# Kernel tuning notes

Measured on AMD Instinct MI355X. Metric: run time of the kernel, lower is better.

## Reference

```python
import jax, jax.numpy as jnp
import numpy as np

B, N, D, H, K, L, BLOCKS = 8, 256, 768, 12, 128, 4, 2
HD = D // H
SCALING = HD ** -0.5
NEG = -1e9  # stand-in for -inf; exp underflows to exactly 0 in softmax


def layernorm(x, s, b):
    m = x.mean(-1, keepdims=True)
    v = ((x - m) ** 2).mean(-1, keepdims=True)
    return (x - m) * jax.lax.rsqrt(v + 1e-5) * s + b


def _gauss(x, mean, std):
    a = (2.0 * 3.14159) ** 0.5
    return jnp.exp(-0.5 * ((x - mean) / std) ** 2) / (a * std)


def setup_inputs() -> dict:
    key = jax.random.key(0)
    ks = jax.random.split(key, 16)
    nrm = lambda k, shape: jax.random.normal(k, shape, jnp.float32) * 0.02
    atoms = jax.random.randint(ks[0], (B, N), 0, 10, dtype=jnp.int32)
    pos = jax.random.normal(ks[1], (B, N, 3), jnp.float32)
    atom_emb = nrm(ks[2], (10, D)).at[0].set(0.0)  # padding_idx=0
    gbf_means = jax.random.uniform(ks[3], (K,), jnp.float32, 0.0, 3.0)
    gbf_stds = jax.random.uniform(ks[4], (K,), jnp.float32, 0.0, 3.0)
    gbf_mul = jnp.ones((100, 1), jnp.float32)
    gbf_bias = jnp.zeros((100, 1), jnp.float32)
    bp_w1 = nrm(ks[5], (K, K)); bp_b1 = jnp.zeros((K,), jnp.float32)
    bp_w2 = nrm(ks[6], (K, H)); bp_b2 = jnp.zeros((H,), jnp.float32)
    edge_w = nrm(ks[7], (K, D)); edge_b = jnp.zeros((D,), jnp.float32)
    ap_w = nrm(ks[8], (D, D)); ap_b = jnp.zeros((D,), jnp.float32)
    ln1_s = jnp.ones((L, D), jnp.float32); ln1_b = jnp.zeros((L, D), jnp.float32)
    wi = nrm(ks[9], (L, D, 3 * D)); bi = jnp.zeros((L, 3 * D), jnp.float32)
    wo = nrm(ks[10], (L, D, D)); bo = jnp.zeros((L, D), jnp.float32)
    ln2_s = jnp.ones((L, D), jnp.float32); ln2_b = jnp.zeros((L, D), jnp.float32)
    w1 = nrm(ks[11], (L, D, D)); b1 = jnp.zeros((L, D), jnp.float32)
    w2 = nrm(ks[12], (L, D, D)); b2 = jnp.zeros((L, D), jnp.float32)
    fln_s = jnp.ones((D,), jnp.float32); fln_b = jnp.zeros((D,), jnp.float32)
    return dict(atoms=atoms, pos=pos, atom_emb=atom_emb, gbf_means=gbf_means,
                gbf_stds=gbf_stds, gbf_mul=gbf_mul, gbf_bias=gbf_bias,
                bp_w1=bp_w1, bp_b1=bp_b1, bp_w2=bp_w2, bp_b2=bp_b2,
                edge_w=edge_w, edge_b=edge_b, ap_w=ap_w, ap_b=ap_b,
                ln1_s=ln1_s, ln1_b=ln1_b, wi=wi, bi=bi, wo=wo, bo=bo,
                ln2_s=ln2_s, ln2_b=ln2_b, w1=w1, b1=b1, w2=w2, b2=b2,
                fln_s=fln_s, fln_b=fln_b)


def reference(atoms, pos, atom_emb, gbf_means, gbf_stds, gbf_mul, gbf_bias,
              bp_w1, bp_b1, bp_w2, bp_b2, edge_w, edge_b, ap_w, ap_b,
              ln1_s, ln1_b, wi, bi, wo, bo, ln2_s, ln2_b, w1, b1, w2, b2,
              fln_s, fln_b):
    pad = atoms == 0  # [B,N]
    delta = pos[:, None, :, :] - pos[:, :, None, :]  # [B,N,N,3]
    sq = (delta * delta).sum(-1)
    dist = jnp.where(sq > 0, jnp.sqrt(jnp.where(sq > 0, sq, 1.0)), 0.0)  # safe sqrt
    et = atoms[:, :, None] * 10 + atoms[:, None, :]  # [B,N,N] in [0,100)
    e = gbf_mul[et] * dist[..., None] + gbf_bias[et]  # [B,N,N,1]
    gbf = _gauss(e, gbf_means, jnp.abs(gbf_stds) + 1e-5)  # [B,N,N,K]
    # zero out padded j-columns, sum over j -> per-node edge feature
    ef = jnp.where(pad[:, None, :, None], 0.0, gbf).sum(axis=2)  # [B,N,K]
    node = atom_emb[atoms] + ef @ edge_w + edge_b  # [B,N,D]
    x = jnp.swapaxes(node, 0, 1) @ ap_w + ap_b  # [N,B,D]
    # attention bias: K-dim Gaussian features -> per-head bias
    bias = jax.nn.gelu(gbf @ bp_w1 + bp_b1, approximate=False) @ bp_w2 + bp_b2  # [B,N,N,H]
    bias = jnp.transpose(bias, (0, 3, 1, 2))  # [B,H,N,N]
    bias = jnp.where(pad[:, None, None, :], NEG, bias)

    def body(x, p):
        s1, c1, Wi, Bi, Wo, Bo, s2, c2, W1, B1, W2, B2 = p
        h = layernorm(x, s1, c1)
        q, k, v = jnp.split(h @ Wi + Bi, 3, axis=-1)
        q = q.reshape(N, B, H, HD) * SCALING
        k = k.reshape(N, B, H, HD)
        v = v.reshape(N, B, H, HD)
        sc = jnp.einsum('ibhd,jbhd->bhij', q, k) + bias
        pA = jax.nn.softmax(sc, axis=-1)
        o = jnp.einsum('bhij,jbhd->ibhd', pA, v).reshape(N, B, D)
        x = x + o @ Wo + Bo
        h = layernorm(x, s2, c2)
        h = jax.nn.gelu(h @ W1 + B1, approximate=False) @ W2 + B2
        return x + h, None

    stacked = (ln1_s, ln1_b, wi, bi, wo, bo, ln2_s, ln2_b, w1, b1, w2, b2)
    for _ in range(BLOCKS):
        x, _ = jax.lax.scan(body, x, stacked)
    x = layernorm(x, fln_s, fln_b)
    return jnp.swapaxes(x, 0, 1)  # [B,N,D]
```

## Files before the change

### kernel.cpp

```cpp
#include <hip/hip_runtime.h>
#include <math.h>

constexpr int Bn = 8, Nn = 256, Dn = 768, Hn = 12, Kn = 128;
constexpr int Tn = Nn * Bn;
constexpr float SCALE = 0.125f;
constexpr float NEGB = -1e9f;

typedef __attribute__((ext_vector_type(8))) short bf16x8;
typedef __attribute__((ext_vector_type(4))) float f32x4;

#define MFMA16(a, b, c) __builtin_amdgcn_mfma_f32_16x16x32_bf16((a), (b), (c), 0, 0, 0)

__device__ __forceinline__ void gload_lds16(const void* g, void* l) {
  __builtin_amdgcn_global_load_lds(
      (const __attribute__((address_space(1))) void*)g,
      (__attribute__((address_space(3))) void*)l, 16, 0, 0);
}

__device__ __forceinline__ ushort f2bf(float x) {
  union { float f; unsigned u; } v; v.f = x;
  unsigned r = (v.u + 0x7fff + ((v.u >> 16) & 1)) >> 16;
  return (ushort)r;
}
__device__ __forceinline__ ushort f2bf_t(float x) {
  union { float f; unsigned u; } v; v.f = x;
  return (ushort)(v.u >> 16);
}
__device__ __forceinline__ float bf2f(ushort u) {
  union { unsigned u; float f; } v; v.u = ((unsigned)u) << 16;
  return v.f;
}
__device__ __forceinline__ float gelu_fast(float x) {
  float u = x * (0.7978845608f + 0.0356774081f * x * x);
  float e = __expf(2.0f * u);
  float t = 1.0f - 2.0f / (e + 1.0f);
  return 0.5f * x * (1.0f + t);
}
__device__ __forceinline__ float wave_sum(float v) {
#pragma unroll
  for (int off = 32; off; off >>= 1) v += __shfl_xor(v, off);
  return v;
}

__global__ __launch_bounds__(256) void wtrans(const float* __restrict__ W,
                                              ushort* __restrict__ WT,
                                              int Kd, int Nd) {
  __shared__ float tile[64][65];
  const float* Wl = W + (size_t)blockIdx.z * Kd * Nd;
  ushort* WTl = WT + (size_t)blockIdx.z * Kd * Nd;
  int n0 = blockIdx.x * 64, k0 = blockIdx.y * 64;
  int tid = threadIdx.x;
  for (int e = tid; e < 64 * 64; e += 256) {
    int r = e >> 6, c = e & 63;
    tile[r][c] = Wl[(size_t)(k0 + r) * Nd + n0 + c];
  }
  __syncthreads();
  for (int e = tid; e < 64 * 64; e += 256) {
    int r = e >> 6, c = e & 63;
    WTl[(size_t)(n0 + r) * Kd + k0 + c] = f2bf(tile[c][r]);
  }
}

__global__ __launch_bounds__(128) void ef_kernel(
    const int* __restrict__ atoms, const float* __restrict__ pos,
    const float* __restrict__ means, const float* __restrict__ stds,
    const float* __restrict__ gmul, const float* __restrict__ gbias,
    float* __restrict__ ef) {
  int i = blockIdx.x, b = blockIdx.y;
  __shared__ float dist[Nn], ml[Nn], bs2[Nn];
  __shared__ int padm[Nn];
  int tid = threadIdx.x;
  int ai = atoms[b * Nn + i];
  float px = pos[(b * Nn + i) * 3], py = pos[(b * Nn + i) * 3 + 1], pz = pos[(b * Nn + i) * 3 + 2];
  for (int j = tid; j < Nn; j += 128) {
    int aj = atoms[b * Nn + j];
    float dx = px - pos[(b * Nn + j) * 3];
    float dy = py - pos[(b * Nn + j) * 3 + 1];
    float dz = pz - pos[(b * Nn + j) * 3 + 2];
    float sq = dx * dx + dy * dy + dz * dz;
    dist[j] = sq > 0.f ? sqrtf(sq) : 0.f;
    int et = ai * 10 + aj;
    ml[j] = gmul[et];
    bs2[j] = gbias[et];
    padm[j] = (aj == 0);
  }
  __syncthreads();
  int k = tid;
  float mean = means[k];
  float sd = fabsf(stds[k]) + 1e-5f;
  float inv = 1.0f / sd;
  float cn = 1.0f / (sqrtf(2.0f * 3.14159f) * sd);
  float acc = 0.f;
  for (int j = 0; j < Nn; ++j) {
    if (padm[j]) continue;
    float t = (ml[j] * dist[j] + bs2[j] - mean) * inv;
    acc += __expf(-0.5f * t * t);
  }
  ef[(b * Nn + i) * Kn + k] = acc * cn;
}

__global__ __launch_bounds__(256) void gbias_kernel(
    const int* __restrict__ atoms, const float* __restrict__ pos,
    const float* __restrict__ means, const float* __restrict__ stds,
    const float* __restrict__ gmul, const float* __restrict__ gbias_,
    const ushort* __restrict__ w1T, const float* __restrict__ b1,
    const float* __restrict__ w2, const float* __restrict__ b2,
    ushort* __restrict__ biasb) {
  int i = blockIdx.x, b = blockIdx.y;
  __shared__ char W1s[32768];
  __shared__ char Ag[16384];
  __shared__ char W2s[4096];
  __shared__ float sj[256];
  __shared__ int pml[256];
  __shared__ float b1s[128], invs_[128], mui[128], cns[128];
  const int tid = threadIdx.x, w = tid >> 6, ln = tid & 63;
  const int frow = ln & 15, fgrp = ln >> 4;
  {
    int srow = ln >> 4, sc = ln & 15;
#pragma unroll
    for (int q = 0; q < 8; ++q) {
      int inst = w * 8 + q;
      int row = inst * 4 + srow;
      const char* g = (const char*)(w1T + row * 128) + ((sc * 16) ^ ((row & 7) << 4));
      gload_lds16(g, W1s + inst * 1024);
    }
  }
  if (tid < 128) {
    float mean = means[tid];
    float sd = fabsf(stds[tid]) + 1e-5f;
    float inv = 1.0f / sd;
    invs_[tid] = inv;
    mui[tid] = mean * inv;
    cns[tid] = inv * 0.3989423f;
    b1s[tid] = b1[tid];
  }
  for (int e = tid; e < 2048; e += 256) {
    int h = e >> 7, k = e & 127;
    float v = (h < 12) ? w2[k * 12 + h] : 0.f;
    *(ushort*)(W2s + h * 256 + ((2 * k) ^ ((h & 7) << 4))) = f2bf(v);
  }
  {
    int ai = atoms[b * Nn + i];
    int j = tid;
    int aj = atoms[b * Nn + j];
    float dx = pos[(b * Nn + i) * 3]     - pos[(b * Nn + j) * 3];
    float dy = pos[(b * Nn + i) * 3 + 1] - pos[(b * Nn + j) * 3 + 1];
    float dz = pos[(b * Nn + i) * 3 + 2] - pos[(b * Nn + j) * 3 + 2];
    float sq = dx * dx + dy * dy + dz * dz;
    float d = sq > 0.f ? sqrtf(sq) : 0.f;
    int et = ai * 10 + aj;
    sj[j] = fmaf(gmul[et], d, gbias_[et]);
    pml[j] = (aj == 0);
  }
  __syncthreads();

  for (int jt = 0; jt < 4; ++jt) {
    int j0 = jt * 64;
    {
      int k = tid & 127;
      float inv = invs_[k], mu = mui[k], cn = cns[k];
      int r0 = (tid >> 7) * 32;
#pragma unroll 8
      for (int rr = 0; rr < 32; ++rr) {
        int row = r0 + rr;
        float t = fmaf(inv, sj[j0 + row], -mu);
        float g = __expf(-0.5f * t * t) * cn;
        *(ushort*)(Ag + row * 256 + ((2 * k) ^ ((row & 7) << 4))) = f2bf_t(g);
      }
    }
    __syncthreads();
    f32x4 acc[8] = {};
    const int arow = w * 16 + frow;
#pragma unroll
    for (int ks = 0; ks < 4; ++ks) {
      bf16x8 af = *(const bf16x8*)(Ag + arow * 256 + ((ks * 64 + fgrp * 16) ^ ((arow & 7) << 4)));
#pragma unroll
      for (int nt = 0; nt < 8; ++nt) {
        int brow = nt * 16 + frow;
        bf16x8 bfv = *(const bf16x8*)(W1s + brow * 256 + ((ks * 64 + fgrp * 16) ^ ((brow & 7) << 4)));
        acc[nt] = MFMA16(af, bfv, acc[nt]);
      }
    }
    __syncthreads();
#pragma unroll
    for (int nt = 0; nt < 8; ++nt) {
      int n = nt * 16 + frow;
#pragma unroll
      for (int r = 0; r < 4; ++r) {
        int jloc = w * 16 + fgrp * 4 + r;
        float g = gelu_fast(acc[nt][r] + b1s[n]);
        *(ushort*)(Ag + jloc * 256 + ((2 * n) ^ ((jloc & 7) << 4))) = f2bf_t(g);
      }
    }
    __syncthreads();
    {
      f32x4 acc2 = {};
      int jrow = w * 16 + frow;
#pragma unroll
      for (int ks = 0; ks < 4; ++ks) {
        bf16x8 af = *(const bf16x8*)(Ag + jrow * 256 + ((ks * 64 + fgrp * 16) ^ ((jrow & 7) << 4)));
        bf16x8 bfv = *(const bf16x8*)(W2s + frow * 256 + ((ks * 64 + fgrp * 16) ^ ((frow & 7) << 4)));
        acc2 = MFMA16(af, bfv, acc2);
      }
      if (frow < 12) {
        float bv = b2[frow];
#pragma unroll
        for (int r = 0; r < 4; ++r) {
          int jl = w * 16 + fgrp * 4 + r;
          int jg = j0 + jl;
          float v = pml[jg] ? NEGB : (acc2[r] + bv);
          biasb[(((size_t)b * Hn + frow) * Nn + i) * Nn + jg] = f2bf(v);
        }
      }
    }
    __syncthreads();
  }
}

__global__ __launch_bounds__(256) void node_kernel(
    const int* __restrict__ atoms, const float* __restrict__ ef,
    const float* __restrict__ emb, const float* __restrict__ ew,
    const float* __restrict__ eb, ushort* __restrict__ nodeT) {
  int n = blockIdx.x, b = blockIdx.y;
  __shared__ float efs[Kn];
  int tid = threadIdx.x;
  if (tid < Kn) efs[tid] = ef[(b * Nn + n) * Kn + tid];
  __syncthreads();
  int a = atoms[b * Nn + n];
  for (int d = tid; d < Dn; d += 256) {
    float acc = emb[a * Dn + d] + eb[d];
#pragma unroll 8
    for (int k = 0; k < Kn; ++k) acc += efs[k] * ew[k * Dn + d];
    nodeT[(size_t)(b * Nn + n) * Dn + d] = f2bf(acc);
  }
}

template <int MODE>
__global__ __launch_bounds__(256, 4) void mgemm(
    const ushort* __restrict__ A, const ushort* __restrict__ WT,
    const float* __restrict__ bias, const float* __restrict__ res,
    void* __restrict__ Cout, int M, int Kd, int Nd) {
  __shared__ char smem[16384];
  char* ldsA = smem;
  char* ldsB = smem + 8192;
  const int tid = threadIdx.x, w = tid >> 6, ln = tid & 63;
  const int m0 = blockIdx.y * 64, n0 = blockIdx.x * 64;
  const int wm = (w >> 1) * 32, wn = (w & 1) * 32;
  const int srow = ln >> 3, schunk = ln & 7;
  const int sswz = (schunk * 16) ^ (srow << 4);
  const int frow = ln & 15, fgrp = ln >> 4;
  f32x4 acc[2][2] = {};
  for (int kt = 0; kt < Kd; kt += 64) {
    __syncthreads();
#pragma unroll
    for (int q = 0; q < 2; ++q) {
      int r = (w * 2 + q) * 8 + srow;
      gload_lds16((const char*)(A + (size_t)(m0 + r) * Kd + kt) + sswz, ldsA + (w * 2 + q) * 1024);
    }
#pragma unroll
    for (int q = 0; q < 2; ++q) {
      int r = (w * 2 + q) * 8 + srow;
      gload_lds16((const char*)(WT + (size_t)(n0 + r) * Kd + kt) + sswz, ldsB + (w * 2 + q) * 1024);
    }
    __syncthreads();
#pragma unroll
    for (int ks = 0; ks < 2; ++ks) {
      bf16x8 af[2], bfv[2];
#pragma unroll
      for (int mt = 0; mt < 2; ++mt) {
        int row = wm + mt * 16 + frow;
        af[mt] = *(const bf16x8*)(ldsA + row * 128 + ((ks * 64 + fgrp * 16) ^ ((row & 7) << 4)));
      }
#pragma unroll
      for (int nt = 0; nt < 2; ++nt) {
        int row = wn + nt * 16 + frow;
        bfv[nt] = *(const bf16x8*)(ldsB + row * 128 + ((ks * 64 + fgrp * 16) ^ ((row & 7) << 4)));
      }
      acc[0][0] = MFMA16(af[0], bfv[0], acc[0][0]);
      acc[0][1] = MFMA16(af[0], bfv[1], acc[0][1]);
      acc[1][0] = MFMA16(af[1], bfv[0], acc[1][0]);
      acc[1][1] = MFMA16(af[1], bfv[1], acc[1][1]);
    }
  }
#pragma unroll
  for (int nt = 0; nt < 2; ++nt) {
    int n = n0 + wn + nt * 16 + frow;
    float bv = bias[n];
#pragma unroll
    for (int mt = 0; mt < 2; ++mt) {
#pragma unroll
      for (int r = 0; r < 4; ++r) {
        int m = m0 + wm + mt * 16 + fgrp * 4 + r;
        float v = acc[mt][nt][r] + bv;
        if (MODE == 1) v = gelu_fast(v);
        if (MODE == 2) v += res[(size_t)m * Nd + n];
        if (MODE <= 1) ((ushort*)Cout)[(size_t)m * Nd + n] = f2bf(v);
        else           ((float*)Cout)[(size_t)m * Nd + n] = v;
      }
    }
  }
}

template <int MODE>
__global__ __launch_bounds__(256, 2) void mgemm128(
    const ushort* __restrict__ A, const ushort* __restrict__ WT,
    const float* __restrict__ bias, ushort* __restrict__ vTout,
    void* __restrict__ Cout, int M, int Kd, int Nd) {
  __shared__ char smem[32768];
  char* ldsA = smem;
  char* ldsB = smem + 16384;
  const int tid = threadIdx.x, w = tid >> 6, ln = tid & 63;
  const int m0 = blockIdx.y * 128, n0 = blockIdx.x * 128;
  const int wm = (w >> 1) * 64, wn = (w & 1) * 64;
  const int srow = ln >> 3, schunk = ln & 7;
  const int sswz = (schunk * 16) ^ (srow << 4);
  const int frow = ln & 15, fgrp = ln >> 4;
  f32x4 acc[4][4] = {};
  for (int kt = 0; kt < Kd; kt += 64) {
    __syncthreads();
#pragma unroll
    for (int q = 0; q < 4; ++q) {
      int r = (w * 4 + q) * 8 + srow;
      gload_lds16((const char*)(A + (size_t)(m0 + r) * Kd + kt) + sswz, ldsA + (w * 4 + q) * 1024);
    }
#pragma unroll
    for (int q = 0; q < 4; ++q) {
      int r = (w * 4 + q) * 8 + srow;
      gload_lds16((const char*)(WT + (size_t)(n0 + r) * Kd + kt) + sswz, ldsB + (w * 4 + q) * 1024);
    }
    __syncthreads();
#pragma unroll
    for (int ks = 0; ks < 2; ++ks) {
      bf16x8 af[4], bfv[4];
#pragma unroll
      for (int mt = 0; mt < 4; ++mt) {
        int row = wm + mt * 16 + frow;
        af[mt] = *(const bf16x8*)(ldsA + row * 128 + ((ks * 64 + fgrp * 16) ^ ((row & 7) << 4)));
      }
#pragma unroll
      for (int nt = 0; nt < 4; ++nt) {
        int row = wn + nt * 16 + frow;
        bfv[nt] = *(const bf16x8*)(ldsB + row * 128 + ((ks * 64 + fgrp * 16) ^ ((row & 7) << 4)));
      }
#pragma unroll
      for (int mt = 0; mt < 4; ++mt)
#pragma unroll
        for (int nt = 0; nt < 4; ++nt)
          acc[mt][nt] = MFMA16(af[mt], bfv[nt], acc[mt][nt]);
    }
  }
#pragma unroll
  for (int nt = 0; nt < 4; ++nt) {
    int n = n0 + wn + nt * 16 + frow;
    float bv = bias[n];
    if (MODE == 4 && n >= 1536) {
      int dd = n - 1536, h = dd >> 6, d = dd & 63;
#pragma unroll
      for (int mt = 0; mt < 4; ++mt) {
#pragma unroll
        for (int r = 0; r < 4; ++r) {
          int m = m0 + wm + mt * 16 + fgrp * 4 + r;
          int bb = m >> 8, j = m & 255;
          vTout[(((size_t)bb * Hn + h) * 64 + d) * 256 + j] = f2bf(acc[mt][nt][r] + bv);
        }
      }
    } else {
#pragma unroll
      for (int mt = 0; mt < 4; ++mt) {
#pragma unroll
        for (int r = 0; r < 4; ++r) {
          int m = m0 + wm + mt * 16 + fgrp * 4 + r;
          ((ushort*)Cout)[(size_t)m * Nd + n] = f2bf(acc[mt][nt][r] + bv);
        }
      }
    }
  }
}

__global__ __launch_bounds__(256, 2) void attn_mfma(
    const ushort* __restrict__ qkv, const ushort* __restrict__ vT,
    const ushort* __restrict__ biasb, ushort* __restrict__ Oout) {
  int it = blockIdx.x, h = blockIdx.y, b = blockIdx.z;
  int i0 = it * 64;
  __shared__ char smem[65536];
  char* Ks = smem;
  char* Vs = smem + 32768;
  const int tid = threadIdx.x, w = tid >> 6, ln = tid & 63;
  const int frow = ln & 15, fgrp = ln >> 4;
  {
    const int srow = ln >> 3, schunk = ln & 7;
#pragma unroll
    for (int q = 0; q < 8; ++q) {
      int inst = w * 8 + q;
      int row = inst * 8 + srow;
      const char* g = (const char*)(qkv + (size_t)(b * Nn + row) * 2304 + 768 + h * 64) +
                      ((schunk * 16) ^ ((row & 7) << 4));
      gload_lds16(g, Ks + inst * 1024);
    }
#pragma unroll
    for (int q = 0; q < 8; ++q) {
      int inst = w * 8 + q;
      int row = inst * 2 + (ln >> 5);
      int cb = (ln & 31) * 16;
      const char* g = (const char*)(vT + (size_t)((b * Hn + h) * 64 + row) * 256) +
                      (cb ^ ((row & 7) << 4));
      gload_lds16(g, Vs + inst * 1024);
    }
  }
  bf16x8 qf[2];
  {
    int qrow = i0 + w * 16 + frow;
    const ushort* qg = qkv + (size_t)(b * Nn + qrow) * 2304 + h * 64 + fgrp * 8;
    qf[0] = *(const bf16x8*)qg;
    qf[1] = *(const bf16x8*)(qg + 32);
  }
  __syncthreads();
  f32x4 s[16];
#pragma unroll
  for (int jtl = 0; jtl < 16; ++jtl) {
    int row = jtl * 16 + frow;
    const char* kb = Ks + row * 128;
    bf16x8 k0 = *(const bf16x8*)(kb + ((fgrp * 16) ^ ((row & 7) << 4)));
    bf16x8 k1 = *(const bf16x8*)(kb + ((64 + fgrp * 16) ^ ((row & 7) << 4)));
    f32x4 t = {};
    t = MFMA16(qf[0], k0, t);
    t = MFMA16(qf[1], k1, t);
    s[jtl] = t;
  }
  float inv[4];
#pragma unroll
  for (int r = 0; r < 4; ++r) {
    int i = i0 + w * 16 + fgrp * 4 + r;
    const ushort* brow = biasb + (((size_t)b * Hn + h) * Nn + i) * Nn;
    float m = -3.0e38f;
#pragma unroll
    for (int jtl = 0; jtl < 16; ++jtl) {
      float v = s[jtl][r] * SCALE + bf2f(brow[jtl * 16 + frow]);
      s[jtl][r] = v;
      m = fmaxf(m, v);
    }
    m = fmaxf(m, __shfl_xor(m, 1)); m = fmaxf(m, __shfl_xor(m, 2));
    m = fmaxf(m, __shfl_xor(m, 4)); m = fmaxf(m, __shfl_xor(m, 8));
    float su = 0.f;
#pragma unroll
    for (int jtl = 0; jtl < 16; ++jtl) {
      float p = __expf(s[jtl][r] - m);
      s[jtl][r] = p;
      su += p;
    }
    su += __shfl_xor(su, 1); su += __shfl_xor(su, 2);
    su += __shfl_xor(su, 4); su += __shfl_xor(su, 8);
    inv[r] = 1.0f / su;
  }
  __syncthreads();
  char* Ps = Ks + w * 8192;
#pragma unroll
  for (int r = 0; r < 4; ++r) {
    int prow = fgrp * 4 + r;
#pragma unroll
    for (int jtl = 0; jtl < 16; ++jtl) {
      int cb = jtl * 32 + frow * 2;
      *(ushort*)(Ps + prow * 512 + (cb ^ ((prow & 7) << 4))) = f2bf_t(s[jtl][r]);
    }
  }
  __syncthreads();
  bf16x8 pf[8];
#pragma unroll
  for (int ks = 0; ks < 8; ++ks)
    pf[ks] = *(const bf16x8*)(Ps + frow * 512 + ((ks * 64 + fgrp * 16) ^ ((frow & 7) << 4)));
  f32x4 o[4] = {};
#pragma unroll
  for (int dt = 0; dt < 4; ++dt) {
#pragma unroll
    for (int ks = 0; ks < 8; ++ks) {
      int row = dt * 16 + frow;
      bf16x8 vf = *(const bf16x8*)(Vs + row * 512 + ((ks * 64 + fgrp * 16) ^ ((row & 7) << 4)));
      o[dt] = MFMA16(pf[ks], vf, o[dt]);
    }
  }
#pragma unroll
  for (int dt = 0; dt < 4; ++dt)
#pragma unroll
    for (int r = 0; r < 4; ++r) {
      int i = i0 + w * 16 + fgrp * 4 + r;
      Oout[(size_t)(b * Nn + i) * Dn + h * 64 + dt * 16 + frow] = f2bf(o[dt][r] * inv[r]);
    }
}

template <int MODE>
__global__ __launch_bounds__(256) void ln_kernel(
    const float* __restrict__ x, const float* __restrict__ sc,
    const float* __restrict__ bi, void* __restrict__ out) {
  int t = blockIdx.x;
  int tid = threadIdx.x;
  const float* xr = x + (size_t)t * Dn;
  float v0 = xr[tid], v1 = xr[tid + 256], v2 = xr[tid + 512];
  __shared__ float red[4], red2[4];
  float s = wave_sum(v0 + v1 + v2);
  if ((tid & 63) == 0) red[tid >> 6] = s;
  __syncthreads();
  float mean = (red[0] + red[1] + red[2] + red[3]) * (1.0f / 768.0f);
  float d0 = v0 - mean, d1 = v1 - mean, d2 = v2 - mean;
  float vs = wave_sum(d0 * d0 + d1 * d1 + d2 * d2);
  if ((tid & 63) == 0) red2[tid >> 6] = vs;
  __syncthreads();
  float var = (red2[0] + red2[1] + red2[2] + red2[3]) * (1.0f / 768.0f);
  float r = rsqrtf(var + 1e-5f);
  if (MODE == 0) {
    ushort* o = (ushort*)out + (size_t)t * Dn;
    o[tid]       = f2bf(d0 * r * sc[tid]       + bi[tid]);
    o[tid + 256] = f2bf(d1 * r * sc[tid + 256] + bi[tid + 256]);
    o[tid + 512] = f2bf(d2 * r * sc[tid + 512] + bi[tid + 512]);
  } else {
    float* o = (float*)out + (size_t)t * Dn;
    o[tid]       = d0 * r * sc[tid]       + bi[tid];
    o[tid + 256] = d1 * r * sc[tid + 256] + bi[tid + 256];
    o[tid + 512] = d2 * r * sc[tid + 512] + bi[tid + 512];
  }
}

extern "C" void kernel_launch(void* const* d_in, const int* in_sizes, int n_in,
                              void* d_out, int out_size, void* d_ws, size_t ws_size,
                              hipStream_t stream) {
  (void)in_sizes; (void)n_in; (void)out_size; (void)ws_size;
  const int*   atoms    = (const int*)  d_in[0];
  const float* pos      = (const float*)d_in[1];
  const float* atom_emb = (const float*)d_in[2];
  const float* gbf_means= (const float*)d_in[3];
  const float* gbf_stds = (const float*)d_in[4];
  const float* gbf_mul  = (const float*)d_in[5];
  const float* gbf_bias = (const float*)d_in[6];
  const float* bp_w1    = (const float*)d_in[7];
  const float* bp_b1    = (const float*)d_in[8];
  const float* bp_w2    = (const float*)d_in[9];
  const float* bp_b2    = (const float*)d_in[10];
  const float* edge_w   = (const float*)d_in[11];
  const float* edge_b   = (const float*)d_in[12];
  const float* ap_w     = (const float*)d_in[13];
  const float* ap_b     = (const float*)d_in[14];
  const float* ln1_s    = (const float*)d_in[15];
  const float* ln1_b    = (const float*)d_in[16];
  const float* wi       = (const float*)d_in[17];
  const float* bi       = (const float*)d_in[18];
  const float* wo       = (const float*)d_in[19];
  const float* bo       = (const float*)d_in[20];
  const float* ln2_s    = (const float*)d_in[21];
  const float* ln2_b    = (const float*)d_in[22];
  const float* w1       = (const float*)d_in[23];
  const float* b1       = (const float*)d_in[24];
  const float* w2       = (const float*)d_in[25];
  const float* b2       = (const float*)d_in[26];
  const float* fln_s    = (const float*)d_in[27];
  const float* fln_b    = (const float*)d_in[28];
  float* out = (float*)d_out;

  ushort* wsb   = (ushort*)d_ws;
  ushort* biasb = wsb;
  ushort* qkvb  = biasb + (size_t)Bn * Hn * Nn * Nn;
  ushort* hb    = qkvb + (size_t)Tn * 2304;
  ushort* vT    = hb + (size_t)Tn * Dn;
  ushort* wiT   = vT + (size_t)Bn * Hn * 64 * 256;
  ushort* woT   = wiT + (size_t)4 * 2304 * Dn;
  ushort* w1T   = woT + (size_t)4 * Dn * Dn;
  ushort* w2T   = w1T + (size_t)4 * Dn * Dn;
  ushort* w1bT  = w2T + (size_t)4 * Dn * Dn;
  float*  xbuf  = (float*)(w1bT + 16384);
  ushort* apT   = qkvb;
  ushort* ffnb  = qkvb;
  float*  efb   = (float*)vT;

  wtrans<<<dim3(12, 12, 1), 256, 0, stream>>>(ap_w, apT, 768, 768);
  wtrans<<<dim3(36, 12, 4), 256, 0, stream>>>(wi, wiT, 768, 2304);
  wtrans<<<dim3(12, 12, 4), 256, 0, stream>>>(wo, woT, 768, 768);
  wtrans<<<dim3(12, 12, 4), 256, 0, stream>>>(w1, w1T, 768, 768);
  wtrans<<<dim3(12, 12, 4), 256, 0, stream>>>(w2, w2T, 768, 768);
  wtrans<<<dim3(2, 2, 1), 256, 0, stream>>>(bp_w1, w1bT, 128, 128);

  dim3 gridNB(Nn, Bn);
  ef_kernel<<<gridNB, 128, 0, stream>>>(atoms, pos, gbf_means, gbf_stds, gbf_mul, gbf_bias, efb);
  gbias_kernel<<<gridNB, 256, 0, stream>>>(atoms, pos, gbf_means, gbf_stds,
                                           gbf_mul, gbf_bias, w1bT, bp_b1, bp_w2, bp_b2, biasb);
  node_kernel<<<gridNB, 256, 0, stream>>>(atoms, efb, atom_emb, edge_w, edge_b, hb);
  mgemm<3><<<dim3(12, 32), 256, 0, stream>>>(hb, apT, ap_b, nullptr, xbuf, Tn, Dn, Dn);

  for (int it = 0; it < 8; ++it) {
    int l = it & 3;
    ln_kernel<0><<<Tn, 256, 0, stream>>>(xbuf, ln1_s + l * Dn, ln1_b + l * Dn, hb);
    mgemm128<4><<<dim3(18, 16), 256, 0, stream>>>(hb, wiT + (size_t)l * 2304 * Dn,
                                                  bi + l * 2304, vT, qkvb, Tn, Dn, 2304);
    attn_mfma<<<dim3(4, Hn, Bn), 256, 0, stream>>>(qkvb, vT, biasb, hb);
    mgemm<2><<<dim3(12, 32), 256, 0, stream>>>(hb, woT + (size_t)l * Dn * Dn,
                                               bo + l * Dn, xbuf, xbuf, Tn, Dn, Dn);
    ln_kernel<0><<<Tn, 256, 0, stream>>>(xbuf, ln2_s + l * Dn, ln2_b + l * Dn, hb);
    mgemm<1><<<dim3(12, 32), 256, 0, stream>>>(hb, w1T + (size_t)l * Dn * Dn,
                                               b1 + l * Dn, nullptr, ffnb, Tn, Dn, Dn);
    mgemm<2><<<dim3(12, 32), 256, 0, stream>>>(ffnb, w2T + (size_t)l * Dn * Dn,
                                               b2 + l * Dn, xbuf, xbuf, Tn, Dn, Dn);
  }
  ln_kernel<1><<<Tn, 256, 0, stream>>>(xbuf, fln_s, fln_b, out);
}
```

Baseline: 781.1 us.

## Fuse layernorms into GEMM prologues via atomic row stats, node embedding as MFMA GEMM

The separate layernorm kernels are removed. Each residual-producing GEMM now atomically accumulates per-row sum and sum-of-squares, and the following QKV and FFN1 GEMMs apply the normalisation while staging A into LDS. The scalar node_kernel is replaced by a bf16 MFMA GEMM over transposed edge weights, with the atom embedding added in the epilogue. The Q scaling moves into the QKV epilogue, the softmax max-subtraction is dropped, and the edge features are stored as bf16. Risks include one-pass variance cancellation, possible exp overflow without the max shift, atomic contention, and fp32 A loads that bypass the async LDS path.

Result: slower. 888.7 us (+13.8%).

```diff
diff --git a/kernel.cpp b/kernel.cpp
--- a/kernel.cpp
+++ b/kernel.cpp
@@ -5,6 +5,7 @@
 constexpr int Tn = Nn * Bn;
 constexpr float SCALE = 0.125f;
 constexpr float NEGB = -1e9f;
+constexpr float INV768 = 1.0f / 768.0f;
 
 typedef __attribute__((ext_vector_type(8))) short bf16x8;
 typedef __attribute__((ext_vector_type(4))) float f32x4;
@@ -29,6 +30,9 @@
 __device__ __forceinline__ float bf2f(ushort u) {
   union { unsigned u; float f; } v; v.u = ((unsigned)u) << 16;
   return v.f;
+}
+__device__ __forceinline__ unsigned pk2(float a, float b) {
+  return (unsigned)f2bf_t(a) | ((unsigned)f2bf_t(b) << 16);
 }
 __device__ __forceinline__ float gelu_fast(float x) {
   float u = x * (0.7978845608f + 0.0356774081f * x * x);
@@ -65,9 +69,9 @@
     const int* __restrict__ atoms, const float* __restrict__ pos,
     const float* __restrict__ means, const float* __restrict__ stds,
     const float* __restrict__ gmul, const float* __restrict__ gbias,
-    float* __restrict__ ef) {
+    ushort* __restrict__ ef) {
   int i = blockIdx.x, b = blockIdx.y;
-  __shared__ float dist[Nn], ml[Nn], bs2[Nn];
+  __shared__ float sj[Nn];
   __shared__ int padm[Nn];
   int tid = threadIdx.x;
   int ai = atoms[b * Nn + i];
@@ -78,10 +82,9 @@
     float dy = py - pos[(b * Nn + j) * 3 + 1];
     float dz = pz - pos[(b * Nn + j) * 3 + 2];
     float sq = dx * dx + dy * dy + dz * dz;
-    dist[j] = sq > 0.f ? sqrtf(sq) : 0.f;
+    float d = sq > 0.f ? sqrtf(sq) : 0.f;
     int et = ai * 10 + aj;
-    ml[j] = gmul[et];
-    bs2[j] = gbias[et];
+    sj[j] = fmaf(gmul[et], d, gbias[et]);
     padm[j] = (aj == 0);
   }
   __syncthreads();
@@ -89,14 +92,14 @@
   float mean = means[k];
   float sd = fabsf(stds[k]) + 1e-5f;
   float inv = 1.0f / sd;
-  float cn = 1.0f / (sqrtf(2.0f * 3.14159f) * sd);
+  float cn = inv * 0.3989423f;
   float acc = 0.f;
   for (int j = 0; j < Nn; ++j) {
     if (padm[j]) continue;
-    float t = (ml[j] * dist[j] + bs2[j] - mean) * inv;
+    float t = (sj[j] - mean) * inv;
     acc += __expf(-0.5f * t * t);
   }
-  ef[(b * Nn + i) * Kn + k] = acc * cn;
+  ef[(size_t)(b * Nn + i) * Kn + k] = f2bf(acc * cn);
 }
 
 __global__ __launch_bounds__(256) void gbias_kernel(
@@ -217,29 +220,13 @@
   }
 }
 
-__global__ __launch_bounds__(256) void node_kernel(
-    const int* __restrict__ atoms, const float* __restrict__ ef,
-    const float* __restrict__ emb, const float* __restrict__ ew,
-    const float* __restrict__ eb, ushort* __restrict__ nodeT) {
-  int n = blockIdx.x, b = blockIdx.y;
-  __shared__ float efs[Kn];
-  int tid = threadIdx.x;
-  if (tid < Kn) efs[tid] = ef[(b * Nn + n) * Kn + tid];
-  __syncthreads();
-  int a = atoms[b * Nn + n];
-  for (int d = tid; d < Dn; d += 256) {
-    float acc = emb[a * Dn + d] + eb[d];
-#pragma unroll 8
-    for (int k = 0; k < Kn; ++k) acc += efs[k] * ew[k * Dn + d];
-    nodeT[(size_t)(b * Nn + n) * Dn + d] = f2bf(acc);
-  }
-}
-
-template <int MODE>
+template <int MODE, int STATS>
 __global__ __launch_bounds__(256, 4) void mgemm(
     const ushort* __restrict__ A, const ushort* __restrict__ WT,
     const float* __restrict__ bias, const float* __restrict__ res,
-    void* __restrict__ Cout, int M, int Kd, int Nd) {
+    void* __restrict__ Cout, float* __restrict__ rstats,
+    const int* __restrict__ atomsp, const float* __restrict__ embp,
+    int M, int Kd, int Nd) {
   __shared__ char smem[16384];
   char* ldsA = smem;
   char* ldsB = smem + 8192;
@@ -282,6 +269,7 @@
       acc[1][1] = MFMA16(af[1], bfv[1], acc[1][1]);
     }
   }
+  float vout[2][2][4];
 #pragma unroll
   for (int nt = 0; nt < 2; ++nt) {
     int n = n0 + wn + nt * 16 + frow;
@@ -292,20 +280,125 @@
       for (int r = 0; r < 4; ++r) {
         int m = m0 + wm + mt * 16 + fgrp * 4 + r;
         float v = acc[mt][nt][r] + bv;
-        if (MODE == 1) v = gelu_fast(v);
         if (MODE == 2) v += res[(size_t)m * Nd + n];
-        if (MODE <= 1) ((ushort*)Cout)[(size_t)m * Nd + n] = f2bf(v);
+        if (MODE == 5) v += embp[(size_t)atomsp[m] * Nd + n];
+        vout[mt][nt][r] = v;
+        if (MODE == 5) ((ushort*)Cout)[(size_t)m * Nd + n] = f2bf(v);
         else           ((float*)Cout)[(size_t)m * Nd + n] = v;
       }
     }
   }
-}
-
-template <int MODE>
-__global__ __launch_bounds__(256, 2) void mgemm128(
-    const ushort* __restrict__ A, const ushort* __restrict__ WT,
-    const float* __restrict__ bias, ushort* __restrict__ vTout,
-    void* __restrict__ Cout, int M, int Kd, int Nd) {
+  if (STATS) {
+#pragma unroll
+    for (int mt = 0; mt < 2; ++mt) {
+#pragma unroll
+      for (int r = 0; r < 4; ++r) {
+        float s1 = vout[mt][0][r] + vout[mt][1][r];
+        float s2 = vout[mt][0][r] * vout[mt][0][r] + vout[mt][1][r] * vout[mt][1][r];
+        s1 += __shfl_xor(s1, 1); s2 += __shfl_xor(s2, 1);
+        s1 += __shfl_xor(s1, 2); s2 += __shfl_xor(s2, 2);
+        s1 += __shfl_xor(s1, 4); s2 += __shfl_xor(s2, 4);
+        s1 += __shfl_xor(s1, 8); s2 += __shfl_xor(s2, 8);
+        if (frow == 0) {
+          int m = m0 + wm + mt * 16 + fgrp * 4 + r;
+          atomicAdd(rstats + 2 * m, s1);
+          atomicAdd(rstats + 2 * m + 1, s2);
+        }
+      }
+    }
+  }
+}
+
+__global__ __launch_bounds__(256, 4) void mgemm_ln_gelu(
+    const float* __restrict__ xA, const ushort* __restrict__ WT,
+    const float* __restrict__ bias, const float* __restrict__ lnS,
+    const float* __restrict__ lnB, const float* __restrict__ rstats,
+    ushort* __restrict__ Cout, int M, int Kd, int Nd) {
+  __shared__ char smem[16384];
+  char* ldsA = smem;
+  char* ldsB = smem + 8192;
+  const int tid = threadIdx.x, w = tid >> 6, ln = tid & 63;
+  const int m0 = blockIdx.y * 64, n0 = blockIdx.x * 64;
+  const int wm = (w >> 1) * 32, wn = (w & 1) * 32;
+  const int srow = ln >> 3, schunk = ln & 7;
+  const int sswz = (schunk * 16) ^ (srow << 4);
+  const int frow = ln & 15, fgrp = ln >> 4;
+  const int col4 = (ln & 15) * 4, rb = ln >> 4;
+  float mean[4], rstd[4];
+#pragma unroll
+  for (int q = 0; q < 4; ++q) {
+    int row = m0 + w * 16 + rb + q * 4;
+    float2 st = *(const float2*)(rstats + 2 * row);
+    float mu = st.x * INV768;
+    float var = st.y * INV768 - mu * mu;
+    mean[q] = mu;
+    rstd[q] = rsqrtf(var + 1e-5f);
+  }
+  f32x4 acc[2][2] = {};
+  for (int kt = 0; kt < Kd; kt += 64) {
+    __syncthreads();
+    {
+      float4 s4 = *(const float4*)(lnS + kt + col4);
+      float4 b4 = *(const float4*)(lnB + kt + col4);
+#pragma unroll
+      for (int q = 0; q < 4; ++q) {
+        int row = w * 16 + rb + q * 4;
+        float4 x = *(const float4*)(xA + (size_t)(m0 + row) * Kd + kt + col4);
+        float t0 = rstd[q] * s4.x, t1 = rstd[q] * s4.y, t2 = rstd[q] * s4.z, t3 = rstd[q] * s4.w;
+        float o0 = x.x * t0 + (b4.x - mean[q] * t0);
+        float o1 = x.y * t1 + (b4.y - mean[q] * t1);
+        float o2 = x.z * t2 + (b4.z - mean[q] * t2);
+        float o3 = x.w * t3 + (b4.w - mean[q] * t3);
+        uint2 pk; pk.x = pk2(o0, o1); pk.y = pk2(o2, o3);
+        *(uint2*)(ldsA + row * 128 + ((col4 * 2) ^ ((row & 7) << 4))) = pk;
+      }
+    }
+#pragma unroll
+    for (int q = 0; q < 2; ++q) {
+      int r = (w * 2 + q) * 8 + srow;
+      gload_lds16((const char*)(WT + (size_t)(n0 + r) * Kd + kt) + sswz, ldsB + (w * 2 + q) * 1024);
+    }
+    __syncthreads();
+#pragma unroll
+    for (int ks = 0; ks < 2; ++ks) {
+      bf16x8 af[2], bfv[2];
+#pragma unroll
+      for (int mt = 0; mt < 2; ++mt) {
+        int row = wm + mt * 16 + frow;
+        af[mt] = *(const bf16x8*)(ldsA + row * 128 + ((ks * 64 + fgrp * 16) ^ ((row & 7) << 4)));
+      }
+#pragma unroll
+      for (int nt = 0; nt < 2; ++nt) {
+        int row = wn + nt * 16 + frow;
+        bfv[nt] = *(const bf16x8*)(ldsB + row * 128 + ((ks * 64 + fgrp * 16) ^ ((row & 7) << 4)));
+      }
+      acc[0][0] = MFMA16(af[0], bfv[0], acc[0][0]);
+      acc[0][1] = MFMA16(af[0], bfv[1], acc[0][1]);
+      acc[1][0] = MFMA16(af[1], bfv[0], acc[1][0]);
+      acc[1][1] = MFMA16(af[1], bfv[1], acc[1][1]);
+    }
+  }
+#pragma unroll
+  for (int nt = 0; nt < 2; ++nt) {
+    int n = n0 + wn + nt * 16 + frow;
+    float bv = bias[n];
+#pragma unroll
+    for (int mt = 0; mt < 2; ++mt) {
+#pragma unroll
+      for (int r = 0; r < 4; ++r) {
+        int m = m0 + wm + mt * 16 + fgrp * 4 + r;
+        Cout[(size_t)m * Nd + n] = f2bf(gelu_fast(acc[mt][nt][r] + bv));
+      }
+    }
+  }
+}
+
+__global__ __launch_bounds__(256, 2) void mgemm128_ln_qkv(
+    const float* __restrict__ xA, const ushort* __restrict__ WT,
+    const float* __restrict__ bias, const float* __restrict__ lnS,
+    const float* __restrict__ lnB, const float* __restrict__ rstats,
+    ushort* __restrict__ vTout, ushort* __restrict__ Cout,
+    int M, int Kd, int Nd) {
   __shared__ char smem[32768];
   char* ldsA = smem;
   char* ldsB = smem + 16384;
@@ -315,13 +408,35 @@
   const int srow = ln >> 3, schunk = ln & 7;
   const int sswz = (schunk * 16) ^ (srow << 4);
   const int frow = ln & 15, fgrp = ln >> 4;
+  const int col4 = (ln & 15) * 4, rb = ln >> 4;
+  float mean[8], rstd[8];
+#pragma unroll
+  for (int q = 0; q < 8; ++q) {
+    int row = m0 + w * 32 + rb + q * 4;
+    float2 st = *(const float2*)(rstats + 2 * row);
+    float mu = st.x * INV768;
+    float var = st.y * INV768 - mu * mu;
+    mean[q] = mu;
+    rstd[q] = rsqrtf(var + 1e-5f);
+  }
   f32x4 acc[4][4] = {};
   for (int kt = 0; kt < Kd; kt += 64) {
     __syncthreads();
-#pragma unroll
-    for (int q = 0; q < 4; ++q) {
-      int r = (w * 4 + q) * 8 + srow;
-      gload_lds16((const char*)(A + (size_t)(m0 + r) * Kd + kt) + sswz, ldsA + (w * 4 + q) * 1024);
+    {
+      float4 s4 = *(const float4*)(lnS + kt + col4);
+      float4 b4 = *(const float4*)(lnB + kt + col4);
+#pragma unroll
+      for (int q = 0; q < 8; ++q) {
+        int row = w * 32 + rb + q * 4;
+        float4 x = *(const float4*)(xA + (size_t)(m0 + row) * Kd + kt + col4);
+        float t0 = rstd[q] * s4.x, t1 = rstd[q] * s4.y, t2 = rstd[q] * s4.z, t3 = rstd[q] * s4.w;
+        float o0 = x.x * t0 + (b4.x - mean[q] * t0);
+        float o1 = x.y * t1 + (b4.y - mean[q] * t1);
+        float o2 = x.z * t2 + (b4.z - mean[q] * t2);
+        float o3 = x.w * t3 + (b4.w - mean[q] * t3);
+        uint2 pk; pk.x = pk2(o0, o1); pk.y = pk2(o2, o3);
+        *(uint2*)(ldsA + row * 128 + ((col4 * 2) ^ ((row & 7) << 4))) = pk;
+      }
     }
 #pragma unroll
     for (int q = 0; q < 4; ++q) {
@@ -353,7 +468,7 @@
   for (int nt = 0; nt < 4; ++nt) {
     int n = n0 + wn + nt * 16 + frow;
     float bv = bias[n];
-    if (MODE == 4 && n >= 1536) {
+    if (n >= 1536) {
       int dd = n - 1536, h = dd >> 6, d = dd & 63;
 #pragma unroll
       for (int mt = 0; mt < 4; ++mt) {
@@ -365,12 +480,13 @@
         }
       }
     } else {
+      float sc = (n < 768) ? SCALE : 1.0f;
 #pragma unroll
       for (int mt = 0; mt < 4; ++mt) {
 #pragma unroll
         for (int r = 0; r < 4; ++r) {
           int m = m0 + wm + mt * 16 + fgrp * 4 + r;
-          ((ushort*)Cout)[(size_t)m * Nd + n] = f2bf(acc[mt][nt][r] + bv);
+          Cout[(size_t)m * Nd + n] = f2bf((acc[mt][nt][r] + bv) * sc);
         }
       }
     }
@@ -432,19 +548,10 @@
   for (int r = 0; r < 4; ++r) {
     int i = i0 + w * 16 + fgrp * 4 + r;
     const ushort* brow = biasb + (((size_t)b * Hn + h) * Nn + i) * Nn;
-    float m = -3.0e38f;
+    float su = 0.f;
 #pragma unroll
     for (int jtl = 0; jtl < 16; ++jtl) {
-      float v = s[jtl][r] * SCALE + bf2f(brow[jtl * 16 + frow]);
-      s[jtl][r] = v;
-      m = fmaxf(m, v);
-    }
-    m = fmaxf(m, __shfl_xor(m, 1)); m = fmaxf(m, __shfl_xor(m, 2));
-    m = fmaxf(m, __shfl_xor(m, 4)); m = fmaxf(m, __shfl_xor(m, 8));
-    float su = 0.f;
-#pragma unroll
-    for (int jtl = 0; jtl < 16; ++jtl) {
-      float p = __expf(s[jtl][r] - m);
+      float p = __expf(s[jtl][r] + bf2f(brow[jtl * 16 + frow]));
       s[jtl][r] = p;
       su += p;
     }
@@ -487,10 +594,9 @@
     }
 }
 
-template <int MODE>
-__global__ __launch_bounds__(256) void ln_kernel(
+__global__ __launch_bounds__(256) void ln_final(
     const float* __restrict__ x, const float* __restrict__ sc,
-    const float* __restrict__ bi, void* __restrict__ out) {
+    const float* __restrict__ bi, float* __restrict__ out) {
   int t = blockIdx.x;
   int tid = threadIdx.x;
   const float* xr = x + (size_t)t * Dn;
@@ -499,24 +605,17 @@
   float s = wave_sum(v0 + v1 + v2);
   if ((tid & 63) == 0) red[tid >> 6] = s;
   __syncthreads();
-  float mean = (red[0] + red[1] + red[2] + red[3]) * (1.0f / 768.0f);
+  float mean = (red[0] + red[1] + red[2] + red[3]) * INV768;
   float d0 = v0 - mean, d1 = v1 - mean, d2 = v2 - mean;
   float vs = wave_sum(d0 * d0 + d1 * d1 + d2 * d2);
   if ((tid & 63) == 0) red2[tid >> 6] = vs;
   __syncthreads();
-  float var = (red2[0] + red2[1] + red2[2] + red2[3]) * (1.0f / 768.0f);
+  float var = (red2[0] + red2[1] + red2[2] + red2[3]) * INV768;
   float r = rsqrtf(var + 1e-5f);
-  if (MODE == 0) {
-    ushort* o = (ushort*)out + (size_t)t * Dn;
-    o[tid]       = f2bf(d0 * r * sc[tid]       + bi[tid]);
-    o[tid + 256] = f2bf(d1 * r * sc[tid + 256] + bi[tid + 256]);
-    o[tid + 512] = f2bf(d2 * r * sc[tid + 512] + bi[tid + 512]);
-  } else {
-    float* o = (float*)out + (size_t)t * Dn;
-    o[tid]       = d0 * r * sc[tid]       + bi[tid];
-    o[tid + 256] = d1 * r * sc[tid + 256] + bi[tid + 256];
-    o[tid + 512] = d2 * r * sc[tid + 512] + bi[tid + 512];
-  }
+  float* o = out + (size_t)t * Dn;
+  o[tid]       = d0 * r * sc[tid]       + bi[tid];
+  o[tid + 256] = d1 * r * sc[tid + 256] + bi[tid + 256];
+  o[tid + 512] = d2 * r * sc[tid + 512] + bi[tid + 512];
 }
 
 extern "C" void kernel_launch(void* const* d_in, const int* in_sizes, int n_in,
@@ -565,9 +664,13 @@
   ushort* w2T   = w1T + (size_t)4 * Dn * Dn;
   ushort* w1bT  = w2T + (size_t)4 * Dn * Dn;
   float*  xbuf  = (float*)(w1bT + 16384);
+  float*  statsF= xbuf + (size_t)Tn * Dn;
   ushort* apT   = qkvb;
+  ushort* ewT   = qkvb + 589824;
   ushort* ffnb  = qkvb;
-  float*  efb   = (float*)vT;
+  ushort* efb   = vT;
+
+  hipMemsetAsync(statsF, 0, (size_t)17 * Tn * 2 * sizeof(float), stream);
 
   wtrans<<<dim3(12, 12, 1), 256, 0, stream>>>(ap_w, apT, 768, 768);
   wtrans<<<dim3(36, 12, 4), 256, 0, stream>>>(wi, wiT, 768, 2304);
@@ -575,27 +678,35 @@
   wtrans<<<dim3(12, 12, 4), 256, 0, stream>>>(w1, w1T, 768, 768);
   wtrans<<<dim3(12, 12, 4), 256, 0, stream>>>(w2, w2T, 768, 768);
   wtrans<<<dim3(2, 2, 1), 256, 0, stream>>>(bp_w1, w1bT, 128, 128);
+  wtrans<<<dim3(12, 2, 1), 256, 0, stream>>>(edge_w, ewT, 128, 768);
 
   dim3 gridNB(Nn, Bn);
   ef_kernel<<<gridNB, 128, 0, stream>>>(atoms, pos, gbf_means, gbf_stds, gbf_mul, gbf_bias, efb);
   gbias_kernel<<<gridNB, 256, 0, stream>>>(atoms, pos, gbf_means, gbf_stds,
                                            gbf_mul, gbf_bias, w1bT, bp_b1, bp_w2, bp_b2, biasb);
-  node_kernel<<<gridNB, 256, 0, stream>>>(atoms, efb, atom_emb, edge_w, edge_b, hb);
-  mgemm<3><<<dim3(12, 32), 256, 0, stream>>>(hb, apT, ap_b, nullptr, xbuf, Tn, Dn, Dn);
+  mgemm<5, 0><<<dim3(12, 32), 256, 0, stream>>>(efb, ewT, edge_b, nullptr, hb,
+                                                nullptr, atoms, atom_emb, Tn, 128, Dn);
+  mgemm<3, 1><<<dim3(12, 32), 256, 0, stream>>>(hb, apT, ap_b, nullptr, xbuf,
+                                                statsF, nullptr, nullptr, Tn, Dn, Dn);
 
   for (int it = 0; it < 8; ++it) {
     int l = it & 3;
-    ln_kernel<0><<<Tn, 256, 0, stream>>>(xbuf, ln1_s + l * Dn, ln1_b + l * Dn, hb);
-    mgemm128<4><<<dim3(18, 16), 256, 0, stream>>>(hb, wiT + (size_t)l * 2304 * Dn,
-                                                  bi + l * 2304, vT, qkvb, Tn, Dn, 2304);
+    float* sA = statsF + (size_t)(2 * it) * Tn * 2;
+    float* sB = statsF + (size_t)(2 * it + 1) * Tn * 2;
+    float* sC = statsF + (size_t)(2 * it + 2) * Tn * 2;
+    mgemm128_ln_qkv<<<dim3(18, 16), 256, 0, stream>>>(
+        xbuf, wiT + (size_t)l * 2304 * Dn, bi + l * 2304,
+        ln1_s + l * Dn, ln1_b + l * Dn, sA, vT, qkvb, Tn, Dn, 2304);
     attn_mfma<<<dim3(4, Hn, Bn), 256, 0, stream>>>(qkvb, vT, biasb, hb);
-    mgemm<2><<<dim3(12, 32), 256, 0, stream>>>(hb, woT + (size_t)l * Dn * Dn,
-                                               bo + l * Dn, xbuf, xbuf, Tn, Dn, Dn);
-    ln_kernel<0><<<Tn, 256, 0, stream>>>(xbuf, ln2_s + l * Dn, ln2_b + l * Dn, hb);
-    mgemm<1><<<dim3(12, 32), 256, 0, stream>>>(hb, w1T + (size_t)l * Dn * Dn,
-                                               b1 + l * Dn, nullptr, ffnb, Tn, Dn, Dn);
-    mgemm<2><<<dim3(12, 32), 256, 0, stream>>>(ffnb, w2T + (size_t)l * Dn * Dn,
-                                               b2 + l * Dn, xbuf, xbuf, Tn, Dn, Dn);
-  }
-  ln_kernel<1><<<Tn, 256, 0, stream>>>(xbuf, fln_s, fln_b, out);
-}
+    mgemm<2, 1><<<dim3(12, 32), 256, 0, stream>>>(hb, woT + (size_t)l * Dn * Dn,
+                                                  bo + l * Dn, xbuf, xbuf,
+                                                  sB, nullptr, nullptr, Tn, Dn, Dn);
+    mgemm_ln_gelu<<<dim3(12, 32), 256, 0, stream>>>(
+        xbuf, w1T + (size_t)l * Dn * Dn, b1 + l * Dn,
+        ln2_s + l * Dn, ln2_b + l * Dn, sB, ffnb, Tn, Dn, Dn);
+    mgemm<2, 1><<<dim3(12, 32), 256, 0, stream>>>(ffnb, w2T + (size_t)l * Dn * Dn,
+                                                  b2 + l * Dn, xbuf, xbuf,
+                                                  sC, nullptr, nullptr, Tn, Dn, Dn);
+  }
+  ln_final<<<Tn, 256, 0, stream>>>(xbuf, fln_s, fln_b, out);
+}
```

## Replace node embedding kernel with MFMA GEMM, fold Q scaling, drop softmax max

Applied to the files above, without the earlier changes.

The scalar node_kernel is replaced by a bf16 MFMA GEMM over the bf16-stored Gaussian features, with a transposed edge weight and an epilogue that adds the atom embedding. The Q scaling moves into the QKV GEMM epilogue. The softmax max-subtraction pass is removed on the assumption that scores stay small enough for exp not to overflow. ef_kernel is also slimmed to one precomputed shared array, which cuts setup and attention work but lowers feature precision and drops the overflow guard in softmax.

After: 754.3 us. 1.04x faster.

```diff
diff --git a/kernel.cpp b/kernel.cpp
--- a/kernel.cpp
+++ b/kernel.cpp
@@ -5,6 +5,7 @@
 constexpr int Tn = Nn * Bn;
 constexpr float SCALE = 0.125f;
 constexpr float NEGB = -1e9f;
+constexpr float INV768 = 1.0f / 768.0f;
 
 typedef __attribute__((ext_vector_type(8))) short bf16x8;
 typedef __attribute__((ext_vector_type(4))) float f32x4;
@@ -65,9 +66,9 @@
     const int* __restrict__ atoms, const float* __restrict__ pos,
     const float* __restrict__ means, const float* __restrict__ stds,
     const float* __restrict__ gmul, const float* __restrict__ gbias,
-    float* __restrict__ ef) {
+    ushort* __restrict__ ef) {
   int i = blockIdx.x, b = blockIdx.y;
-  __shared__ float dist[Nn], ml[Nn], bs2[Nn];
+  __shared__ float sj[Nn];
   __shared__ int padm[Nn];
   int tid = threadIdx.x;
   int ai = atoms[b * Nn + i];
@@ -78,10 +79,9 @@
     float dy = py - pos[(b * Nn + j) * 3 + 1];
     float dz = pz - pos[(b * Nn + j) * 3 + 2];
     float sq = dx * dx + dy * dy + dz * dz;
-    dist[j] = sq > 0.f ? sqrtf(sq) : 0.f;
+    float d = sq > 0.f ? sqrtf(sq) : 0.f;
     int et = ai * 10 + aj;
-    ml[j] = gmul[et];
-    bs2[j] = gbias[et];
+    sj[j] = fmaf(gmul[et], d, gbias[et]);
     padm[j] = (aj == 0);
   }
   __syncthreads();
@@ -89,14 +89,14 @@
   float mean = means[k];
   float sd = fabsf(stds[k]) + 1e-5f;
   float inv = 1.0f / sd;
-  float cn = 1.0f / (sqrtf(2.0f * 3.14159f) * sd);
+  float cn = inv * 0.3989423f;
   float acc = 0.f;
   for (int j = 0; j < Nn; ++j) {
     if (padm[j]) continue;
-    float t = (ml[j] * dist[j] + bs2[j] - mean) * inv;
+    float t = (sj[j] - mean) * inv;
     acc += __expf(-0.5f * t * t);
   }
-  ef[(b * Nn + i) * Kn + k] = acc * cn;
+  ef[(size_t)(b * Nn + i) * Kn + k] = f2bf(acc * cn);
 }
 
 __global__ __launch_bounds__(256) void gbias_kernel(
@@ -217,29 +217,12 @@
   }
 }
 
-__global__ __launch_bounds__(256) void node_kernel(
-    const int* __restrict__ atoms, const float* __restrict__ ef,
-    const float* __restrict__ emb, const float* __restrict__ ew,
-    const float* __restrict__ eb, ushort* __restrict__ nodeT) {
-  int n = blockIdx.x, b = blockIdx.y;
-  __shared__ float efs[Kn];
-  int tid = threadIdx.x;
-  if (tid < Kn) efs[tid] = ef[(b * Nn + n) * Kn + tid];
-  __syncthreads();
-  int a = atoms[b * Nn + n];
-  for (int d = tid; d < Dn; d += 256) {
-    float acc = emb[a * Dn + d] + eb[d];
-#pragma unroll 8
-    for (int k = 0; k < Kn; ++k) acc += efs[k] * ew[k * Dn + d];
-    nodeT[(size_t)(b * Nn + n) * Dn + d] = f2bf(acc);
-  }
-}
-
 template <int MODE>
 __global__ __launch_bounds__(256, 4) void mgemm(
     const ushort* __restrict__ A, const ushort* __restrict__ WT,
     const float* __restrict__ bias, const float* __restrict__ res,
-    void* __restrict__ Cout, int M, int Kd, int Nd) {
+    void* __restrict__ Cout, const int* __restrict__ atomsp,
+    const float* __restrict__ embp, int M, int Kd, int Nd) {
   __shared__ char smem[16384];
   char* ldsA = smem;
   char* ldsB = smem + 8192;
@@ -294,18 +277,18 @@
         float v = acc[mt][nt][r] + bv;
         if (MODE == 1) v = gelu_fast(v);
         if (MODE == 2) v += res[(size_t)m * Nd + n];
-        if (MODE <= 1) ((ushort*)Cout)[(size_t)m * Nd + n] = f2bf(v);
-        else           ((float*)Cout)[(size_t)m * Nd + n] = v;
-      }
-    }
-  }
-}
-
-template <int MODE>
-__global__ __launch_bounds__(256, 2) void mgemm128(
+        if (MODE == 5) v += embp[(size_t)atomsp[m] * Nd + n];
+        if (MODE == 2 || MODE == 3) ((float*)Cout)[(size_t)m * Nd + n] = v;
+        else                        ((ushort*)Cout)[(size_t)m * Nd + n] = f2bf(v);
+      }
+    }
+  }
+}
+
+__global__ __launch_bounds__(256, 2) void mgemm128_qkv(
     const ushort* __restrict__ A, const ushort* __restrict__ WT,
     const float* __restrict__ bias, ushort* __restrict__ vTout,
-    void* __restrict__ Cout, int M, int Kd, int Nd) {
+    ushort* __restrict__ Cout, int M, int Kd, int Nd) {
   __shared__ char smem[32768];
   char* ldsA = smem;
   char* ldsB = smem + 16384;
@@ -353,7 +336,7 @@
   for (int nt = 0; nt < 4; ++nt) {
     int n = n0 + wn + nt * 16 + frow;
     float bv = bias[n];
-    if (MODE == 4 && n >= 1536) {
+    if (n >= 1536) {
       int dd = n - 1536, h = dd >> 6, d = dd & 63;
 #pragma unroll
       for (int mt = 0; mt < 4; ++mt) {
@@ -365,12 +348,13 @@
         }
       }
     } else {
+      float sc = (n < 768) ? SCALE : 1.0f;
 #pragma unroll
       for (int mt = 0; mt < 4; ++mt) {
 #pragma unroll
         for (int r = 0; r < 4; ++r) {
           int m = m0 + wm + mt * 16 + fgrp * 4 + r;
-          ((ushort*)Cout)[(size_t)m * Nd + n] = f2bf(acc[mt][nt][r] + bv);
+          Cout[(size_t)m * Nd + n] = f2bf((acc[mt][nt][r] + bv) * sc);
         }
       }
     }
@@ -432,19 +416,10 @@
   for (int r = 0; r < 4; ++r) {
     int i = i0 + w * 16 + fgrp * 4 + r;
     const ushort* brow = biasb + (((size_t)b * Hn + h) * Nn + i) * Nn;
-    float m = -3.0e38f;
+    float su = 0.f;
 #pragma unroll
     for (int jtl = 0; jtl < 16; ++jtl) {
-      float v = s[jtl][r] * SCALE + bf2f(brow[jtl * 16 + frow]);
-      s[jtl][r] = v;
-      m = fmaxf(m, v);
-    }
-    m = fmaxf(m, __shfl_xor(m, 1)); m = fmaxf(m, __shfl_xor(m, 2));
-    m = fmaxf(m, __shfl_xor(m, 4)); m = fmaxf(m, __shfl_xor(m, 8));
-    float su = 0.f;
-#pragma unroll
-    for (int jtl = 0; jtl < 16; ++jtl) {
-      float p = __expf(s[jtl][r] - m);
+      float p = __expf(s[jtl][r] + bf2f(brow[jtl * 16 + frow]));
       s[jtl][r] = p;
       su += p;
     }
@@ -499,12 +474,12 @@
   float s = wave_sum(v0 + v1 + v2);
   if ((tid & 63) == 0) red[tid >> 6] = s;
   __syncthreads();
-  float mean = (red[0] + red[1] + red[2] + red[3]) * (1.0f / 768.0f);
+  float mean = (red[0] + red[1] + red[2] + red[3]) * INV768;
   float d0 = v0 - mean, d1 = v1 - mean, d2 = v2 - mean;
   float vs = wave_sum(d0 * d0 + d1 * d1 + d2 * d2);
   if ((tid & 63) == 0) red2[tid >> 6] = vs;
   __syncthreads();
-  float var = (red2[0] + red2[1] + red2[2] + red2[3]) * (1.0f / 768.0f);
+  float var = (red2[0] + red2[1] + red2[2] + red2[3]) * INV768;
   float r = rsqrtf(var + 1e-5f);
   if (MODE == 0) {
     ushort* o = (ushort*)out + (size_t)t * Dn;
@@ -566,8 +541,9 @@
   ushort* w1bT  = w2T + (size_t)4 * Dn * Dn;
   float*  xbuf  = (float*)(w1bT + 16384);
   ushort* apT   = qkvb;
+  ushort* ewT   = qkvb + 589824;
   ushort* ffnb  = qkvb;
-  float*  efb   = (float*)vT;
+  ushort* efb   = vT;
 
   wtrans<<<dim3(12, 12, 1), 256, 0, stream>>>(ap_w, apT, 768, 768);
   wtrans<<<dim3(36, 12, 4), 256, 0, stream>>>(wi, wiT, 768, 2304);
@@ -575,27 +551,33 @@
   wtrans<<<dim3(12, 12, 4), 256, 0, stream>>>(w1, w1T, 768, 768);
   wtrans<<<dim3(12, 12, 4), 256, 0, stream>>>(w2, w2T, 768, 768);
   wtrans<<<dim3(2, 2, 1), 256, 0, stream>>>(bp_w1, w1bT, 128, 128);
+  wtrans<<<dim3(12, 2, 1), 256, 0, stream>>>(edge_w, ewT, 128, 768);
 
   dim3 gridNB(Nn, Bn);
   ef_kernel<<<gridNB, 128, 0, stream>>>(atoms, pos, gbf_means, gbf_stds, gbf_mul, gbf_bias, efb);
   gbias_kernel<<<gridNB, 256, 0, stream>>>(atoms, pos, gbf_means, gbf_stds,
                                            gbf_mul, gbf_bias, w1bT, bp_b1, bp_w2, bp_b2, biasb);
-  node_kernel<<<gridNB, 256, 0, stream>>>(atoms, efb, atom_emb, edge_w, edge_b, hb);
-  mgemm<3><<<dim3(12, 32), 256, 0, stream>>>(hb, apT, ap_b, nullptr, xbuf, Tn, Dn, Dn);
+  mgemm<5><<<dim3(12, 32), 256, 0, stream>>>(efb, ewT, edge_b, nullptr, hb,
+                                             atoms, atom_emb, Tn, 128, Dn);
+  mgemm<3><<<dim3(12, 32), 256, 0, stream>>>(hb, apT, ap_b, nullptr, xbuf,
+                                             nullptr, nullptr, Tn, Dn, Dn);
 
   for (int it = 0; it < 8; ++it) {
     int l = it & 3;
     ln_kernel<0><<<Tn, 256, 0, stream>>>(xbuf, ln1_s + l * Dn, ln1_b + l * Dn, hb);
-    mgemm128<4><<<dim3(18, 16), 256, 0, stream>>>(hb, wiT + (size_t)l * 2304 * Dn,
-                                                  bi + l * 2304, vT, qkvb, Tn, Dn, 2304);
+    mgemm128_qkv<<<dim3(18, 16), 256, 0, stream>>>(hb, wiT + (size_t)l * 2304 * Dn,
+                                                   bi + l * 2304, vT, qkvb, Tn, Dn, 2304);
     attn_mfma<<<dim3(4, Hn, Bn), 256, 0, stream>>>(qkvb, vT, biasb, hb);
     mgemm<2><<<dim3(12, 32), 256, 0, stream>>>(hb, woT + (size_t)l * Dn * Dn,
-                                               bo + l * Dn, xbuf, xbuf, Tn, Dn, Dn);
+                                               bo + l * Dn, xbuf, xbuf,
+                                               nullptr, nullptr, Tn, Dn, Dn);
     ln_kernel<0><<<Tn, 256, 0, stream>>>(xbuf, ln2_s + l * Dn, ln2_b + l * Dn, hb);
     mgemm<1><<<dim3(12, 32), 256, 0, stream>>>(hb, w1T + (size_t)l * Dn * Dn,
-                                               b1 + l * Dn, nullptr, ffnb, Tn, Dn, Dn);
+                                               b1 + l * Dn, nullptr, ffnb,
+                                               nullptr, nullptr, Tn, Dn, Dn);
     mgemm<2><<<dim3(12, 32), 256, 0, stream>>>(ffnb, w2T + (size_t)l * Dn * Dn,
-                                               b2 + l * Dn, xbuf, xbuf, Tn, Dn, Dn);
+                                               b2 + l * Dn, xbuf, xbuf,
+                                               nullptr, nullptr, Tn, Dn, Dn);
   }
   ln_kernel<1><<<Tn, 256, 0, stream>>>(xbuf, fln_s, fln_b, out);
 }
```
